# Optimization experiments

Hardware: AMD Instinct MI355X
Metric: run time of the kernel (lower is better)

The kernel has to match this reference:

```python
import jax, jax.numpy as jnp
import numpy as np

N = 100_000      # nodes
E = 1_600_000    # edges
F_IN = 128       # node_features
H1, H2 = 50, 20  # GCLSTM hidden sizes (fixed in the model)


def _norm_weights(src, dst, w, n):
    # PyG get_laplacian(sym): remove self loops, deg over row, sym-normalize.
    w = jnp.where(src == dst, jnp.zeros_like(w), w)  # remove self-loops (weight 0)
    deg = jax.ops.segment_sum(w, src, num_segments=n)
    deg_safe = jnp.where(deg > 0, deg, jnp.ones_like(deg))
    dis = jnp.where(deg > 0, deg_safe ** -0.5, jnp.zeros_like(deg))
    return dis[src] * w * dis[dst]


def _lhat_matvec(x, src, dst, wn, n):
    # L_hat = 2*L/lambda_max - I with sym norm and lambda_max=2  =>  -D^-1/2 A D^-1/2
    return -jax.ops.segment_sum(wn[:, None] * x[src], dst, num_segments=n)


def _gclstm_cell(x, src, dst, wn, n, Wx, bx, theta, bconv, out_ch):
    # One GCLSTM step with H = C = 0 (the model passes H=C=None).
    H = jnp.zeros((n, out_ch), x.dtype)
    C = jnp.zeros((n, out_ch), x.dtype)
    # ChebConv(H) for all 4 gates: Tx_0 = H, Tx_1 = L_hat @ H   (K = 2)
    Tx = jnp.stack([H, _lhat_matvec(H, src, dst, wn, n)])       # [2, n, out]
    conv = jnp.einsum('knf,gkfo->gno', Tx, theta) + bconv[:, None, :]  # [4, n, out]
    Z = x @ Wx + bx                                              # [n, 4*out], gates i,f,c,o
    zi, zf, zc, zo = jnp.split(Z, 4, axis=-1)
    I = jax.nn.sigmoid(zi + conv[0])
    Fg = jax.nn.sigmoid(zf + conv[1])
    T = jnp.tanh(zc + conv[2])
    C = Fg * C + I * T
    O = jax.nn.sigmoid(zo + conv[3])
    return O * jnp.tanh(C)


def setup_inputs() -> dict:
    key = jax.random.key(0)
    ks = jax.random.split(key, 14)
    s = 0.1  # param init scale
    return {
        'x': jax.random.normal(ks[0], (N, F_IN), jnp.float32),
        'edge_index': jax.random.randint(ks[1], (2, E), 0, N, dtype=jnp.int32),
        'edge_weight': jax.random.uniform(ks[2], (E,), jnp.float32),
        # layer 1: W_x for gates i,f,c,o concatenated, Cheb thetas [gate, K, in, out]
        'Wx1': s * jax.random.normal(ks[3], (F_IN, 4 * H1), jnp.float32),
        'bx1': s * jax.random.normal(ks[4], (4 * H1,), jnp.float32),
        'theta1': s * jax.random.normal(ks[5], (4, 2, H1, H1), jnp.float32),
        'bconv1': s * jax.random.normal(ks[6], (4, H1), jnp.float32),
        # layer 2
        'Wx2': s * jax.random.normal(ks[7], (H1, 4 * H2), jnp.float32),
        'bx2': s * jax.random.normal(ks[8], (4 * H2,), jnp.float32),
        'theta2': s * jax.random.normal(ks[9], (4, 2, H2, H2), jnp.float32),
        'bconv2': s * jax.random.normal(ks[10], (4, H2), jnp.float32),
        # linear head
        'Wl': s * jax.random.normal(ks[11], (H2, 1), jnp.float32),
        'bl': s * jax.random.normal(ks[12], (1,), jnp.float32),
    }


def reference(x, edge_index, edge_weight, Wx1, bx1, theta1, bconv1,
              Wx2, bx2, theta2, bconv2, Wl, bl):
    src, dst = edge_index[0], edge_index[1]
    wn = _norm_weights(src, dst, edge_weight, N)
    h = _gclstm_cell(x, src, dst, wn, N, Wx1, bx1, theta1, bconv1, H1)
    h = _gclstm_cell(h, src, dst, wn, N, Wx2, bx2, theta2, bconv2, H2)
    h = jax.nn.relu(h)
    # F.dropout: identity at inference (deterministic baseline)
    return h @ Wl + bl  # [N, 1]
```

## Files before the change

### kernel.cpp

```cpp
#include <hip/hip_runtime.h>
#include <hip/hip_bf16.h>


#define NODES 100000
#define NTILES 6250
#define GRID_BLOCKS 512
#define WAVES_TOTAL 2048

typedef float v4f   __attribute__((ext_vector_type(4)));
typedef float fragC __attribute__((ext_vector_type(4)));
typedef short frag8 __attribute__((ext_vector_type(8)));

#define OFF_B1H 0
#define OFF_B2H 40960
#define OFF_PB1 49152
#define OFF_PB2 49792

__device__ __forceinline__ unsigned short f2bf(float f) {
  unsigned int u = __float_as_uint(f);
  u += 0x7fffu + ((u >> 16) & 1u);
  return (unsigned short)(u >> 16);
}
__device__ __forceinline__ float fsig(float z) {
  float t = __builtin_amdgcn_exp2f(z * -1.44269504088896f);
  return __builtin_amdgcn_rcpf(1.0f + t);
}
__device__ __forceinline__ float ftanh(float z) {
  float t = __builtin_amdgcn_exp2f(z * 2.88539008177793f);
  return 1.0f - 2.0f * __builtin_amdgcn_rcpf(t + 1.0f);
}

union bfu { __hip_bfloat162 h; unsigned int u; };

__device__ __forceinline__ void cvt8(const float* v, frag8& hi, frag8& lo) {
  float lof[8];
#pragma unroll
  for (int p = 0; p < 4; ++p) {
    bfu c; c.h = __float22bfloat162_rn(make_float2(v[2 * p], v[2 * p + 1]));
    hi[2 * p]     = (short)(c.u & 0xffffu);
    hi[2 * p + 1] = (short)(c.u >> 16);
    lof[2 * p]     = v[2 * p]     - __uint_as_float((c.u & 0xffffu) << 16);
    lof[2 * p + 1] = v[2 * p + 1] - __uint_as_float(c.u & 0xffff0000u);
  }
#pragma unroll
  for (int p = 0; p < 4; ++p) {
    bfu c; c.h = __float22bfloat162_rn(make_float2(lof[2 * p], lof[2 * p + 1]));
    lo[2 * p]     = (short)(c.u & 0xffffu);
    lo[2 * p + 1] = (short)(c.u >> 16);
  }
}

__global__ void pack_weights(const float* __restrict__ Wx1, const float* __restrict__ bx1,
                             const float* __restrict__ bconv1,
                             const float* __restrict__ Wx2, const float* __restrict__ bx2,
                             const float* __restrict__ bconv2,
                             unsigned char* __restrict__ ws) {
  const int tid = blockIdx.x * blockDim.x + threadIdx.x;
  const int stride = gridDim.x * blockDim.x;
  unsigned short* B1H = (unsigned short*)(ws + OFF_B1H);
  unsigned short* B2H = (unsigned short*)(ws + OFF_B2H);
  float* PB1 = (float*)(ws + OFF_PB1);
  float* PB2 = (float*)(ws + OFF_PB2);

  for (int idx = tid; idx < 20480; idx += stride) {
    int j = idx & 7, lane = (idx >> 3) & 63, ft = idx >> 9;
    int s = ft / 10, t = ft % 10;
    int k = 32 * s + ((lane >> 4) << 3) + j;
    int m = lane & 15;
    int c = -1, g = 0;
    if (t <= 8) { g = t % 3; c = 16 * (t / 3) + m; }
    else if (m < 6) { c = 48 + m / 3; g = m % 3; }
    float val = 0.f;
    if (c >= 0) {
      int gs = (g == 0) ? 0 : (g == 1) ? 2 : 3;
      val = Wx1[k * 200 + gs * 50 + c];
    }
    B1H[idx] = f2bf(val);
  }
  for (int idx = tid; idx < 4096; idx += stride) {
    int j = idx & 7, lane = (idx >> 3) & 63, ft = idx >> 9;
    int s = ft >> 2, t = ft & 3;
    int k = 32 * s + ((lane >> 4) << 3) + j;
    int m = lane & 15;
    int c = -1, g = 0;
    if (t <= 2) { g = t; c = m; }
    else if (m < 12) { c = 16 + m / 3; g = m % 3; }
    float val = 0.f;
    if (c >= 0 && k < 50) {
      int gs = (g == 0) ? 0 : (g == 1) ? 2 : 3;
      val = Wx2[k * 80 + gs * 20 + c];
    }
    B2H[idx] = f2bf(val);
  }
  for (int idx = tid; idx < 160; idx += stride) {
    int t = idx >> 4, m = idx & 15;
    int c = -1, g = 0;
    if (t <= 8) { g = t % 3; c = 16 * (t / 3) + m; }
    else if (m < 6) { c = 48 + m / 3; g = m % 3; }
    float v = 0.f;
    if (c >= 0) {
      int gs = (g == 0) ? 0 : (g == 1) ? 2 : 3;
      v = bx1[gs * 50 + c] + bconv1[gs * 50 + c];
    }
    PB1[idx] = v;
  }
  for (int idx = tid; idx < 64; idx += stride) {
    int t = idx >> 4, m = idx & 15;
    int c = -1, g = 0;
    if (t <= 2) { g = t; c = m; }
    else if (m < 12) { c = 16 + m / 3; g = m % 3; }
    float v = 0.f;
    if (c >= 0) {
      int gs = (g == 0) ? 0 : (g == 1) ? 2 : 3;
      v = bx2[gs * 20 + c] + bconv2[gs * 20 + c];
    }
    PB2[idx] = v;
  }
}

__global__ __launch_bounds__(256, 2) void gclstm_main(
    const float* __restrict__ x, const unsigned char* __restrict__ wsb,
    const float* __restrict__ Wl, const float* __restrict__ bl,
    float* __restrict__ out) {
  __shared__ short sB1[20480];
  __shared__ short sB2[4096];
  __shared__ unsigned short sH[4][16 * 72];
  __shared__ float sPB1[160];
  __shared__ float sPB2[64];

  const int tid = threadIdx.x;
  const int lane = tid & 63;
  const int wave = tid >> 6;
  const int m = lane & 15;
  const int q = lane >> 4;

  {
    const v4f* g1 = (const v4f*)(wsb + OFF_B1H);
    v4f* s1 = (v4f*)sB1;
    for (int i = tid; i < 2560; i += 256) s1[i] = g1[i];
    const v4f* g2 = (const v4f*)(wsb + OFF_B2H);
    v4f* s2 = (v4f*)sB2;
    for (int i = tid; i < 512; i += 256) s2[i] = g2[i];
    const float* p1 = (const float*)(wsb + OFF_PB1);
    if (tid < 160) sPB1[tid] = p1[tid];
    const float* p2 = (const float*)(wsb + OFF_PB2);
    if (tid < 64) sPB2[tid] = p2[tid];
    unsigned int* hz = (unsigned int*)sH;
    for (int i = tid; i < 2304; i += 256) hz[i] = 0u;
  }
  __syncthreads();

  const float wlm = Wl[m];
  const float wlx = (m < 4) ? Wl[16 + m] : 0.f;
  const float blv = bl[0];

  unsigned short* sHw = (unsigned short*)sH + wave * (16 * 72);
  const frag8* sB1f = (const frag8*)sB1;
  const frag8* sB2f = (const frag8*)sB2;
  const int gw = blockIdx.x * 4 + wave;

  v4f abuf[8];
  int tau = gw;
  {
    const float* xr = x + (size_t)(tau * 16 + m) * 128 + q * 8;
#pragma unroll
    for (int s = 0; s < 4; ++s) {
      abuf[2 * s] = *(const v4f*)(xr + 32 * s);
      abuf[2 * s + 1] = *(const v4f*)(xr + 32 * s + 4);
    }
  }

  for (; tau < NTILES; tau += WAVES_TOTAL) {
    frag8 ah[4], al[4];
#pragma unroll
    for (int s = 0; s < 4; ++s) {
      float av[8];
      *(v4f*)av = abuf[2 * s];
      *(v4f*)(av + 4) = abuf[2 * s + 1];
      cvt8(av, ah[s], al[s]);
    }
    int tn = tau + WAVES_TOTAL;
    if (tn < NTILES) {
      const float* xr = x + (size_t)(tn * 16 + m) * 128 + q * 8;
#pragma unroll
      for (int s = 0; s < 4; ++s) {
        abuf[2 * s] = *(const v4f*)(xr + 32 * s);
        abuf[2 * s + 1] = *(const v4f*)(xr + 32 * s + 4);
      }
    }

    fragC acc[10];
#pragma unroll
    for (int t = 0; t < 10; ++t) {
      float bv = sPB1[16 * t + m];
      acc[t] = (fragC){bv, bv, bv, bv};
    }
#pragma unroll
    for (int s = 0; s < 4; ++s) {
#pragma unroll
      for (int t = 0; t < 10; ++t) {
        frag8 b = sB1f[(s * 10 + t) * 64 + lane];
        acc[t] = __builtin_amdgcn_mfma_f32_16x16x32_bf16(ah[s], b, acc[t], 0, 0, 0);
        acc[t] = __builtin_amdgcn_mfma_f32_16x16x32_bf16(al[s], b, acc[t], 0, 0, 0);
      }
      __builtin_amdgcn_sched_barrier(0);
    }

#pragma unroll
    for (int b = 0; b < 3; ++b)
#pragma unroll
      for (int r = 0; r < 4; ++r) {
        float I = fsig(acc[3 * b][r]);
        float T = ftanh(acc[3 * b + 1][r]);
        float O = fsig(acc[3 * b + 2][r]);
        sHw[(q * 4 + r) * 72 + 16 * b + m] = f2bf(O * ftanh(I * T));
      }
#pragma unroll
    for (int r = 0; r < 4; ++r) {
      float vI = __shfl(acc[9][r], 16 * q + m);
      float vT = __shfl(acc[9][r], 16 * q + m + 1);
      float vO = __shfl(acc[9][r], 16 * q + m + 2);
      if (m == 0 || m == 3) {
        float I = fsig(vI), T = ftanh(vT), O = fsig(vO);
        sHw[(q * 4 + r) * 72 + 48 + (m >> 1)] = f2bf(O * ftanh(I * T));
      }
    }

    frag8 hh[2];
#pragma unroll
    for (int s = 0; s < 2; ++s)
      hh[s] = *(const frag8*)(sHw + m * 72 + 32 * s + 8 * q);
    fragC acc2[4];
#pragma unroll
    for (int t = 0; t < 4; ++t) {
      float bv = sPB2[16 * t + m];
      acc2[t] = (fragC){bv, bv, bv, bv};
    }
#pragma unroll
    for (int s = 0; s < 2; ++s)
#pragma unroll
      for (int t = 0; t < 4; ++t) {
        frag8 b = sB2f[(s * 4 + t) * 64 + lane];
        acc2[t] = __builtin_amdgcn_mfma_f32_16x16x32_bf16(hh[s], b, acc2[t], 0, 0, 0);
      }

    v4f res;
#pragma unroll
    for (int r = 0; r < 4; ++r) {
      float I = fsig(acc2[0][r]);
      float T = ftanh(acc2[1][r]);
      float O = fsig(acc2[2][r]);
      float h2 = O * ftanh(I * T);
      float part = fmaxf(h2, 0.f) * wlm;
      float eI = __shfl(acc2[3][r], 16 * q + 3 * m);
      float eT = __shfl(acc2[3][r], 16 * q + 3 * m + 1);
      float eO = __shfl(acc2[3][r], 16 * q + 3 * m + 2);
      float I2 = fsig(eI), T2 = ftanh(eT), O2 = fsig(eO);
      float h2x = O2 * ftanh(I2 * T2);
      part += fmaxf(h2x, 0.f) * wlx;
      part += __shfl_xor(part, 1);
      part += __shfl_xor(part, 2);
      part += __shfl_xor(part, 4);
      part += __shfl_xor(part, 8);
      res[r] = part + blv;
    }
    if (m == 0) *(v4f*)(out + tau * 16 + 4 * q) = res;
  }
}

extern "C" void kernel_launch(void* const* d_in, const int* in_sizes, int n_in,
                              void* d_out, int out_size, void* d_ws, size_t ws_size,
                              hipStream_t stream) {
  (void)in_sizes; (void)n_in; (void)out_size; (void)ws_size;
  const float* x = (const float*)d_in[0];
  const float* Wx1 = (const float*)d_in[3];
  const float* bx1 = (const float*)d_in[4];
  const float* bconv1 = (const float*)d_in[6];
  const float* Wx2 = (const float*)d_in[7];
  const float* bx2 = (const float*)d_in[8];
  const float* bconv2 = (const float*)d_in[10];
  const float* Wl = (const float*)d_in[11];
  const float* bl = (const float*)d_in[12];
  unsigned char* ws = (unsigned char*)d_ws;

  hipLaunchKernelGGL(pack_weights, dim3(32), dim3(256), 0, stream,
                     Wx1, bx1, bconv1, Wx2, bx2, bconv2, ws);
  hipLaunchKernelGGL(gclstm_main, dim3(GRID_BLOCKS), dim3(256), 0, stream,
                     x, ws, Wl, bl, (float*)d_out);
}
```

Before: 132.6 us.

## Replace persistent grid-stride loop with one tile per wave launch

```diff
diff --git a/kernel.cpp b/kernel.cpp
--- a/kernel.cpp
+++ b/kernel.cpp
@@ -4,8 +4,6 @@
 
 #define NODES 100000
 #define NTILES 6250
-#define GRID_BLOCKS 512
-#define WAVES_TOTAL 2048
 
 typedef float v4f   __attribute__((ext_vector_type(4)));
 typedef float fragC __attribute__((ext_vector_type(4)));
@@ -118,12 +116,11 @@
   }
 }
 
-__global__ __launch_bounds__(256, 2) void gclstm_main(
+__global__ __launch_bounds__(256) void gclstm_main(
     const float* __restrict__ x, const unsigned char* __restrict__ wsb,
     const float* __restrict__ Wl, const float* __restrict__ bl,
     float* __restrict__ out) {
   __shared__ short sB1[20480];
-  __shared__ short sB2[4096];
   __shared__ unsigned short sH[4][16 * 72];
   __shared__ float sPB1[160];
   __shared__ float sPB2[64];
@@ -133,14 +130,12 @@
   const int wave = tid >> 6;
   const int m = lane & 15;
   const int q = lane >> 4;
+  const int tau = blockIdx.x * 4 + wave;
 
   {
     const v4f* g1 = (const v4f*)(wsb + OFF_B1H);
     v4f* s1 = (v4f*)sB1;
     for (int i = tid; i < 2560; i += 256) s1[i] = g1[i];
-    const v4f* g2 = (const v4f*)(wsb + OFF_B2H);
-    v4f* s2 = (v4f*)sB2;
-    for (int i = tid; i < 512; i += 256) s2[i] = g2[i];
     const float* p1 = (const float*)(wsb + OFF_PB1);
     if (tid < 160) sPB1[tid] = p1[tid];
     const float* p2 = (const float*)(wsb + OFF_PB2);
@@ -150,122 +145,104 @@
   }
   __syncthreads();
 
+  if (tau >= NTILES) return;
+
+  unsigned short* sHw = (unsigned short*)sH + wave * (16 * 72);
+  const frag8* sB1f = (const frag8*)sB1;
+
+  const float* xr = x + (size_t)(tau * 16 + m) * 128 + q * 8;
+  v4f xb[8];
+#pragma unroll
+  for (int s = 0; s < 4; ++s) {
+    xb[2 * s] = *(const v4f*)(xr + 32 * s);
+    xb[2 * s + 1] = *(const v4f*)(xr + 32 * s + 4);
+  }
+
+  fragC acc[10];
+#pragma unroll
+  for (int t = 0; t < 10; ++t) {
+    float bv = sPB1[16 * t + m];
+    acc[t] = (fragC){bv, bv, bv, bv};
+  }
+#pragma unroll
+  for (int s = 0; s < 4; ++s) {
+    float av[8];
+    *(v4f*)av = xb[2 * s];
+    *(v4f*)(av + 4) = xb[2 * s + 1];
+    frag8 ah, al;
+    cvt8(av, ah, al);
+#pragma unroll
+    for (int t = 0; t < 10; ++t) {
+      frag8 b = sB1f[(s * 10 + t) * 64 + lane];
+      acc[t] = __builtin_amdgcn_mfma_f32_16x16x32_bf16(ah, b, acc[t], 0, 0, 0);
+      acc[t] = __builtin_amdgcn_mfma_f32_16x16x32_bf16(al, b, acc[t], 0, 0, 0);
+    }
+    __builtin_amdgcn_sched_barrier(0);
+  }
+
+#pragma unroll
+  for (int b = 0; b < 3; ++b)
+#pragma unroll
+    for (int r = 0; r < 4; ++r) {
+      float I = fsig(acc[3 * b][r]);
+      float T = ftanh(acc[3 * b + 1][r]);
+      float O = fsig(acc[3 * b + 2][r]);
+      sHw[(q * 4 + r) * 72 + 16 * b + m] = f2bf(O * ftanh(I * T));
+    }
+#pragma unroll
+  for (int r = 0; r < 4; ++r) {
+    float vI = __shfl(acc[9][r], 16 * q + m);
+    float vT = __shfl(acc[9][r], 16 * q + m + 1);
+    float vO = __shfl(acc[9][r], 16 * q + m + 2);
+    if (m == 0 || m == 3) {
+      float I = fsig(vI), T = ftanh(vT), O = fsig(vO);
+      sHw[(q * 4 + r) * 72 + 48 + (m >> 1)] = f2bf(O * ftanh(I * T));
+    }
+  }
+
+  const frag8* g2 = (const frag8*)(wsb + OFF_B2H);
+  frag8 hh[2];
+#pragma unroll
+  for (int s = 0; s < 2; ++s)
+    hh[s] = *(const frag8*)(sHw + m * 72 + 32 * s + 8 * q);
+  fragC acc2[4];
+#pragma unroll
+  for (int t = 0; t < 4; ++t) {
+    float bv = sPB2[16 * t + m];
+    acc2[t] = (fragC){bv, bv, bv, bv};
+  }
+#pragma unroll
+  for (int s = 0; s < 2; ++s)
+#pragma unroll
+    for (int t = 0; t < 4; ++t) {
+      frag8 b = g2[(s * 4 + t) * 64 + lane];
+      acc2[t] = __builtin_amdgcn_mfma_f32_16x16x32_bf16(hh[s], b, acc2[t], 0, 0, 0);
+    }
+
   const float wlm = Wl[m];
   const float wlx = (m < 4) ? Wl[16 + m] : 0.f;
   const float blv = bl[0];
-
-  unsigned short* sHw = (unsigned short*)sH + wave * (16 * 72);
-  const frag8* sB1f = (const frag8*)sB1;
-  const frag8* sB2f = (const frag8*)sB2;
-  const int gw = blockIdx.x * 4 + wave;
-
-  v4f abuf[8];
-  int tau = gw;
-  {
-    const float* xr = x + (size_t)(tau * 16 + m) * 128 + q * 8;
-#pragma unroll
-    for (int s = 0; s < 4; ++s) {
-      abuf[2 * s] = *(const v4f*)(xr + 32 * s);
-      abuf[2 * s + 1] = *(const v4f*)(xr + 32 * s + 4);
-    }
-  }
-
-  for (; tau < NTILES; tau += WAVES_TOTAL) {
-    frag8 ah[4], al[4];
-#pragma unroll
-    for (int s = 0; s < 4; ++s) {
-      float av[8];
-      *(v4f*)av = abuf[2 * s];
-      *(v4f*)(av + 4) = abuf[2 * s + 1];
-      cvt8(av, ah[s], al[s]);
-    }
-    int tn = tau + WAVES_TOTAL;
-    if (tn < NTILES) {
-      const float* xr = x + (size_t)(tn * 16 + m) * 128 + q * 8;
-#pragma unroll
-      for (int s = 0; s < 4; ++s) {
-        abuf[2 * s] = *(const v4f*)(xr + 32 * s);
-        abuf[2 * s + 1] = *(const v4f*)(xr + 32 * s + 4);
-      }
-    }
-
-    fragC acc[10];
-#pragma unroll
-    for (int t = 0; t < 10; ++t) {
-      float bv = sPB1[16 * t + m];
-      acc[t] = (fragC){bv, bv, bv, bv};
-    }
-#pragma unroll
-    for (int s = 0; s < 4; ++s) {
-#pragma unroll
-      for (int t = 0; t < 10; ++t) {
-        frag8 b = sB1f[(s * 10 + t) * 64 + lane];
-        acc[t] = __builtin_amdgcn_mfma_f32_16x16x32_bf16(ah[s], b, acc[t], 0, 0, 0);
-        acc[t] = __builtin_amdgcn_mfma_f32_16x16x32_bf16(al[s], b, acc[t], 0, 0, 0);
-      }
-      __builtin_amdgcn_sched_barrier(0);
-    }
-
-#pragma unroll
-    for (int b = 0; b < 3; ++b)
-#pragma unroll
-      for (int r = 0; r < 4; ++r) {
-        float I = fsig(acc[3 * b][r]);
-        float T = ftanh(acc[3 * b + 1][r]);
-        float O = fsig(acc[3 * b + 2][r]);
-        sHw[(q * 4 + r) * 72 + 16 * b + m] = f2bf(O * ftanh(I * T));
-      }
-#pragma unroll
-    for (int r = 0; r < 4; ++r) {
-      float vI = __shfl(acc[9][r], 16 * q + m);
-      float vT = __shfl(acc[9][r], 16 * q + m + 1);
-      float vO = __shfl(acc[9][r], 16 * q + m + 2);
-      if (m == 0 || m == 3) {
-        float I = fsig(vI), T = ftanh(vT), O = fsig(vO);
-        sHw[(q * 4 + r) * 72 + 48 + (m >> 1)] = f2bf(O * ftanh(I * T));
-      }
-    }
-
-    frag8 hh[2];
-#pragma unroll
-    for (int s = 0; s < 2; ++s)
-      hh[s] = *(const frag8*)(sHw + m * 72 + 32 * s + 8 * q);
-    fragC acc2[4];
-#pragma unroll
-    for (int t = 0; t < 4; ++t) {
-      float bv = sPB2[16 * t + m];
-      acc2[t] = (fragC){bv, bv, bv, bv};
-    }
-#pragma unroll
-    for (int s = 0; s < 2; ++s)
-#pragma unroll
-      for (int t = 0; t < 4; ++t) {
-        frag8 b = sB2f[(s * 4 + t) * 64 + lane];
-        acc2[t] = __builtin_amdgcn_mfma_f32_16x16x32_bf16(hh[s], b, acc2[t], 0, 0, 0);
-      }
-
-    v4f res;
-#pragma unroll
-    for (int r = 0; r < 4; ++r) {
-      float I = fsig(acc2[0][r]);
-      float T = ftanh(acc2[1][r]);
-      float O = fsig(acc2[2][r]);
-      float h2 = O * ftanh(I * T);
-      float part = fmaxf(h2, 0.f) * wlm;
-      float eI = __shfl(acc2[3][r], 16 * q + 3 * m);
-      float eT = __shfl(acc2[3][r], 16 * q + 3 * m + 1);
-      float eO = __shfl(acc2[3][r], 16 * q + 3 * m + 2);
-      float I2 = fsig(eI), T2 = ftanh(eT), O2 = fsig(eO);
-      float h2x = O2 * ftanh(I2 * T2);
-      part += fmaxf(h2x, 0.f) * wlx;
-      part += __shfl_xor(part, 1);
-      part += __shfl_xor(part, 2);
-      part += __shfl_xor(part, 4);
-      part += __shfl_xor(part, 8);
-      res[r] = part + blv;
-    }
-    if (m == 0) *(v4f*)(out + tau * 16 + 4 * q) = res;
-  }
+  v4f res;
+#pragma unroll
+  for (int r = 0; r < 4; ++r) {
+    float I = fsig(acc2[0][r]);
+    float T = ftanh(acc2[1][r]);
+    float O = fsig(acc2[2][r]);
+    float h2 = O * ftanh(I * T);
+    float part = fmaxf(h2, 0.f) * wlm;
+    float eI = __shfl(acc2[3][r], 16 * q + 3 * m);
+    float eT = __shfl(acc2[3][r], 16 * q + 3 * m + 1);
+    float eO = __shfl(acc2[3][r], 16 * q + 3 * m + 2);
+    float I2 = fsig(eI), T2 = ftanh(eT), O2 = fsig(eO);
+    float h2x = O2 * ftanh(I2 * T2);
+    part += fmaxf(h2x, 0.f) * wlx;
+    part += __shfl_xor(part, 1);
+    part += __shfl_xor(part, 2);
+    part += __shfl_xor(part, 4);
+    part += __shfl_xor(part, 8);
+    res[r] = part + blv;
+  }
+  if (m == 0) *(v4f*)(out + tau * 16 + 4 * q) = res;
 }
 
 extern "C" void kernel_launch(void* const* d_in, const int* in_sizes, int n_in,
@@ -285,6 +262,6 @@
 
   hipLaunchKernelGGL(pack_weights, dim3(32), dim3(256), 0, stream,
                      Wx1, bx1, bconv1, Wx2, bx2, bconv2, ws);
-  hipLaunchKernelGGL(gclstm_main, dim3(GRID_BLOCKS), dim3(256), 0, stream,
+  hipLaunchKernelGGL(gclstm_main, dim3((NTILES + 3) / 4), dim3(256), 0, stream,
                      x, ws, Wl, bl, (float*)d_out);
 }
```

New measurement: 134.7 us. No clear change (+1.5%).
